# Kernel tuning notes

Hardware: AMD Instinct MI355X
Metric: run time of the kernel (lower is better)

## Reference

```python
import jax, jax.numpy as jnp
import numpy as np
from jax import lax

B, C, H, W = 32, 256, 56, 56
EPS = 1e-5


def ste_sign(x):
    # Binarize with clipped straight-through estimator (ReActNet style):
    # forward = sign(x), backward = 1 where |x| < 1.
    c = jnp.clip(x, -1.0, 1.0)
    return c + lax.stop_gradient(jnp.sign(x) - c)


def rsign(x, beta):
    # per-channel learnable shift then binarize; beta: [C]
    return ste_sign(x - beta[None, :, None, None])


def scaled_sign_weight(w):
    # w: [Cout, Cin, k, k] -> alpha * sign(w), alpha = mean|w| per filter
    alpha = jnp.mean(jnp.abs(w), axis=(1, 2, 3), keepdims=True)
    sw = w + lax.stop_gradient(jnp.sign(w) - w)  # STE through sign
    return alpha * sw


def conv2d(x, w, padding):
    return lax.conv_general_dilated(
        x, w, window_strides=(1, 1), padding=[(padding, padding)] * 2,
        dimension_numbers=("NCHW", "OIHW", "NCHW"))


def bn(x, g, b, m, v):
    inv = g / jnp.sqrt(v + EPS)
    return x * inv[None, :, None, None] + (b - m * inv)[None, :, None, None]


def rprelu(x, gamma, slope, zeta):
    # RPReLU: PReLU(x - gamma) + zeta, all per-channel
    y = x - gamma[None, :, None, None]
    return jnp.where(y > 0, y, slope[None, :, None, None] * y) + zeta[None, :, None, None]


def setup_inputs() -> dict:
    key = jax.random.key(0)
    ks = jax.random.split(key, 12)
    return {
        "x": jax.random.normal(ks[0], (B, C, H, W), jnp.float32),
        "rsign1_beta": jax.random.normal(ks[1], (C,), jnp.float32) * 0.1,
        "w1": jax.random.normal(ks[2], (C, C, 3, 3), jnp.float32) * 0.05,
        "bn1_g": jnp.ones((C,), jnp.float32),
        "bn1_b": jnp.zeros((C,), jnp.float32),
        "bn1_m": jax.random.normal(ks[3], (C,), jnp.float32) * 0.1,
        "bn1_v": jax.random.uniform(ks[4], (C,), jnp.float32) + 0.5,
        "rsign2_beta": jax.random.normal(ks[5], (C,), jnp.float32) * 0.1,
        "w2": jax.random.normal(ks[6], (C, C, 1, 1), jnp.float32) * 0.05,
        "bn2_g": jnp.ones((C,), jnp.float32),
        "bn2_b": jnp.zeros((C,), jnp.float32),
        "bn2_m": jax.random.normal(ks[7], (C,), jnp.float32) * 0.1,
        "bn2_v": jax.random.uniform(ks[8], (C,), jnp.float32) + 0.5,
        "pr_gamma": jax.random.normal(ks[9], (C,), jnp.float32) * 0.1,
        "pr_slope": jnp.full((C,), 0.25, jnp.float32),
        "pr_zeta": jax.random.normal(ks[10], (C,), jnp.float32) * 0.1,
    }


def reference(x, rsign1_beta, w1, bn1_g, bn1_b, bn1_m, bn1_v,
              rsign2_beta, w2, bn2_g, bn2_b, bn2_m, bn2_v,
              pr_gamma, pr_slope, pr_zeta):
    # layer1: RSign -> binarized 3x3 conv -> BN, + residual, RPReLU
    out = bn(conv2d(rsign(x, rsign1_beta), scaled_sign_weight(w1), 1),
             bn1_g, bn1_b, bn1_m, bn1_v)
    out = out + x
    out_r = rprelu(out, pr_gamma, pr_slope, pr_zeta)
    # layer2: RSign -> binarized 1x1 conv -> BN, + residual, RPReLU (shared params)
    out = bn(conv2d(rsign(out_r, rsign2_beta), scaled_sign_weight(w2), 0),
             bn2_g, bn2_b, bn2_m, bn2_v)
    out = out + out_r
    return rprelu(out, pr_gamma, pr_slope, pr_zeta)
```

## Files before the change

### kernel.cpp

```cpp
#include <hip/hip_runtime.h>
#include <stdint.h>

#define BB 32
#define CC_ 256
#define HH 56
#define WW 56
#define TW 28
#define TCOLS 30
#define EPSV 1e-5f

typedef unsigned long long u64;

__global__ __launch_bounds__(256) void prep_weights(
    const float* __restrict__ w1, const float* __restrict__ w2,
    const float* __restrict__ bn1_g, const float* __restrict__ bn1_b,
    const float* __restrict__ bn1_m, const float* __restrict__ bn1_v,
    const float* __restrict__ bn2_g, const float* __restrict__ bn2_b,
    const float* __restrict__ bn2_m, const float* __restrict__ bn2_v,
    u64* __restrict__ pw1, u64* __restrict__ pw2,
    float* __restrict__ scale1, float* __restrict__ shift1,
    float* __restrict__ scale2, float* __restrict__ shift2)
{
    int co = blockIdx.x;
    int ci = threadIdx.x;
    int wv = ci >> 6, lane = ci & 63;

    float wvals[9];
    const float* wp = w1 + ((size_t)co*256 + ci)*9;
    float s1 = 0.f;
#pragma unroll
    for (int t = 0; t < 9; ++t) { wvals[t] = wp[t]; s1 += fabsf(wvals[t]); }
    float v2 = w2[(size_t)co*256 + ci];
    float s2 = fabsf(v2);

#pragma unroll
    for (int t = 0; t < 9; ++t) {
        u64 b = __ballot(wvals[t] > 0.0f);
        if (lane == 0) pw1[((size_t)co*9 + t)*4 + wv] = b;
    }
    {
        u64 b = __ballot(v2 > 0.0f);
        if (lane == 0) pw2[(size_t)co*4 + wv] = b;
    }

    for (int off = 32; off > 0; off >>= 1) {
        s1 += __shfl_down(s1, off);
        s2 += __shfl_down(s2, off);
    }
    __shared__ float r1[4], r2[4];
    if (lane == 0) { r1[wv] = s1; r2[wv] = s2; }
    __syncthreads();
    if (ci == 0) {
        float a1 = (r1[0]+r1[1]+r1[2]+r1[3]) * (1.0f/2304.0f);
        float a2 = (r2[0]+r2[1]+r2[2]+r2[3]) * (1.0f/256.0f);
        float inv1 = bn1_g[co] / sqrtf(bn1_v[co] + EPSV);
        float inv2 = bn2_g[co] / sqrtf(bn2_v[co] + EPSV);
        scale1[co] = a1 * inv1;
        shift1[co] = bn1_b[co] - bn1_m[co]*inv1;
        scale2[co] = a2 * inv2;
        shift2[co] = bn2_b[co] - bn2_m[co]*inv2;
    }
}

__global__ __launch_bounds__(256) void pack_input(
    const float* __restrict__ x, const float* __restrict__ beta1,
    u64* __restrict__ pack1)
{
    __shared__ float xrow[CC_][WW+1];
    int bid = blockIdx.x;
    int n = bid / HH, h = bid % HH;
    int tid = threadIdx.x;

    for (int idx = tid; idx < CC_*14; idx += 256) {
        int c = idx / 14, g = idx - c*14;
        float4 v = *(const float4*)(x + (((size_t)n*CC_ + c)*HH + h)*WW + 4*g);
        xrow[c][4*g+0] = v.x; xrow[c][4*g+1] = v.y;
        xrow[c][4*g+2] = v.z; xrow[c][4*g+3] = v.w;
    }
    __syncthreads();

    int wv = tid >> 6, lane = tid & 63;
    float beta = beta1[wv*64 + lane];
    u64 mine = 0;
    for (int ww = 0; ww < WW; ++ww) {
        u64 b = __ballot(xrow[wv*64 + lane][ww] > beta);
        if (ww == lane) mine = b;
    }
    if (lane < WW) pack1[((size_t)bid*WW + lane)*4 + wv] = mine;
}

__device__ __forceinline__ int tap_pop(const u64* __restrict__ col, const u64* __restrict__ wr) {
    ulonglong2 a = *(const ulonglong2*)(col);
    ulonglong2 b = *(const ulonglong2*)(col + 2);
    return __builtin_popcountll(a.x ^ wr[0]) + __builtin_popcountll(a.y ^ wr[1])
         + __builtin_popcountll(b.x ^ wr[2]) + __builtin_popcountll(b.y ^ wr[3]);
}

__global__ __launch_bounds__(256, 4) void main_fused(
    const float* __restrict__ x,
    const u64* __restrict__ pack1,
    const u64* __restrict__ pw1, const u64* __restrict__ pw2,
    const float* __restrict__ scale1, const float* __restrict__ shift1,
    const float* __restrict__ scale2, const float* __restrict__ shift2,
    const float* __restrict__ beta2,
    const float* __restrict__ pr_gamma, const float* __restrict__ pr_slope,
    const float* __restrict__ pr_zeta,
    float* __restrict__ out)
{
    __shared__ u64 rows[3][TCOLS][4];
    __shared__ float outr[CC_][TW+1];
    __shared__ u64 p2[TW][4];

    int bid = blockIdx.x;
    int tile = bid & 1;
    int nh = bid >> 1;
    int n = nh / HH, h = nh % HH;
    int w0 = tile * TW;
    int tid = threadIdx.x;
    int wv = tid >> 6;
    int lane = tid & 63;
    int cc = tid;

    u64 wr1[36];
    {
        const u64* wq1 = pw1 + (size_t)cc*36;
#pragma unroll
        for (int j = 0; j < 18; ++j) {
            ulonglong2 v = *(const ulonglong2*)(wq1 + 2*j);
            wr1[2*j] = v.x; wr1[2*j+1] = v.y;
        }
    }
    u64 wr2[4];
    {
        ulonglong2 a = *(const ulonglong2*)(pw2 + (size_t)cc*4);
        ulonglong2 b = *(const ulonglong2*)(pw2 + (size_t)cc*4 + 2);
        wr2[0]=a.x; wr2[1]=a.y; wr2[2]=b.x; wr2[3]=b.y;
    }
    float sc1 = scale1[cc], sh1 = shift1[cc];
    float sc2 = scale2[cc], sh2 = shift2[cc];
    float gam = pr_gamma[cc], slp = pr_slope[cc], zet = pr_zeta[cc];
    float bet2 = beta2[cc];

    {
        int hm = (h > 0) ? h-1 : 0;
        int hp = (h < HH-1) ? h+1 : HH-1;
        for (int idx = tid; idx < 3*TCOLS*4; idx += 256) {
            int r = idx / (TCOLS*4);
            int rem = idx - r*(TCOLS*4);
            int j = rem >> 2, q = rem & 3;
            int gw = w0 - 1 + j;
            gw = (gw < 0) ? 0 : ((gw > WW-1) ? WW-1 : gw);
            int hr = (r == 0) ? hm : ((r == 1) ? h : hp);
            rows[r][j][q] = pack1[((size_t)(n*HH + hr)*WW + gw)*4 + q];
        }
    }
    for (int idx = tid; idx < CC_*7; idx += 256) {
        int c = idx / 7, g = idx - c*7;
        float4 v = *(const float4*)(x + (((size_t)n*CC_ + c)*HH + h)*WW + w0 + 4*g);
        outr[c][4*g+0] = v.x; outr[c][4*g+1] = v.y;
        outr[c][4*g+2] = v.z; outr[c][4*g+3] = v.w;
    }
    __syncthreads();

    bool rowU = (h > 0), rowD = (h < HH-1);

    if (rowU && rowD) {
        int pstart = 0, pend = TW;
        if (tile == 0) {
            int acc = 0;
#pragma unroll
            for (int r = 0; r < 3; ++r) {
                acc += tap_pop(&rows[r][1][0], &wr1[(r*3+1)*4]);
                acc += tap_pop(&rows[r][2][0], &wr1[(r*3+2)*4]);
            }
            float s = (float)(1536 - 2*acc);
            float y = fmaf(s, sc1, sh1) + outr[cc][0];
            float yr = y - gam;
            outr[cc][0] = fmaf(slp, fminf(yr, 0.f), fmaxf(yr, 0.f)) + zet;
            pstart = 1;
        } else {
            int acc = 0;
#pragma unroll
            for (int r = 0; r < 3; ++r) {
                acc += tap_pop(&rows[r][TW-1][0], &wr1[(r*3+0)*4]);
                acc += tap_pop(&rows[r][TW][0],   &wr1[(r*3+1)*4]);
            }
            float s = (float)(1536 - 2*acc);
            float y = fmaf(s, sc1, sh1) + outr[cc][TW-1];
            float yr = y - gam;
            outr[cc][TW-1] = fmaf(slp, fminf(yr, 0.f), fmaxf(yr, 0.f)) + zet;
            pend = TW-1;
        }
        for (int p = pstart; p < pend; ++p) {
            int acc = 0;
#pragma unroll
            for (int r = 0; r < 3; ++r) {
#pragma unroll
                for (int dc = 0; dc < 3; ++dc)
                    acc += tap_pop(&rows[r][p+dc][0], &wr1[(r*3+dc)*4]);
            }
            float s = (float)(2304 - 2*acc);
            float y = fmaf(s, sc1, sh1) + outr[cc][p];
            float yr = y - gam;
            outr[cc][p] = fmaf(slp, fminf(yr, 0.f), fmaxf(yr, 0.f)) + zet;
        }
    } else {
        for (int p = 0; p < TW; ++p) {
            int w = w0 + p;
            bool colL = (w > 0), colR = (w < WW-1);
            int acc = 0, nval = 0;
#pragma unroll
            for (int t = 0; t < 9; ++t) {
                int r = t / 3, dc = t - 3*r;
                bool v = ((r == 0) ? rowU : (r == 2) ? rowD : true)
                      && ((dc == 0) ? colL : (dc == 2) ? colR : true);
                if (v) { acc += tap_pop(&rows[r][p+dc][0], &wr1[t*4]); ++nval; }
            }
            float s = (float)(256*nval - 2*acc);
            float y = fmaf(s, sc1, sh1) + outr[cc][p];
            float yr = y - gam;
            outr[cc][p] = fmaf(slp, fminf(yr, 0.f), fmaxf(yr, 0.f)) + zet;
        }
    }

    {
        u64 mine = 0;
        for (int ww = 0; ww < TW; ++ww) {
            u64 b = __ballot(outr[cc][ww] > bet2);
            if (ww == lane) mine = b;
        }
        if (lane < TW) p2[lane][wv] = mine;
    }
    __syncthreads();

    for (int p = 0; p < TW; ++p) {
        ulonglong2 a = *(const ulonglong2*)&p2[p][0];
        ulonglong2 b = *(const ulonglong2*)&p2[p][2];
        int pc = __builtin_popcountll(a.x ^ wr2[0]) + __builtin_popcountll(a.y ^ wr2[1])
               + __builtin_popcountll(b.x ^ wr2[2]) + __builtin_popcountll(b.y ^ wr2[3]);
        float s = (float)(256 - 2*pc);
        float y = fmaf(s, sc2, sh2) + outr[cc][p];
        float yr = y - gam;
        outr[cc][p] = fmaf(slp, fminf(yr, 0.f), fmaxf(yr, 0.f)) + zet;
    }
    __syncthreads();

    for (int idx = tid; idx < CC_*7; idx += 256) {
        int c = idx / 7, g = idx - c*7;
        float4 v;
        v.x = outr[c][4*g+0]; v.y = outr[c][4*g+1];
        v.z = outr[c][4*g+2]; v.w = outr[c][4*g+3];
        *(float4*)(out + (((size_t)n*CC_ + c)*HH + h)*WW + w0 + 4*g) = v;
    }
}

extern "C" void kernel_launch(void* const* d_in, const int* in_sizes, int n_in,
                              void* d_out, int out_size, void* d_ws, size_t ws_size,
                              hipStream_t stream) {
    const float* x           = (const float*)d_in[0];
    const float* rsign1_beta = (const float*)d_in[1];
    const float* w1          = (const float*)d_in[2];
    const float* bn1_g       = (const float*)d_in[3];
    const float* bn1_b       = (const float*)d_in[4];
    const float* bn1_m       = (const float*)d_in[5];
    const float* bn1_v       = (const float*)d_in[6];
    const float* rsign2_beta = (const float*)d_in[7];
    const float* w2          = (const float*)d_in[8];
    const float* bn2_g       = (const float*)d_in[9];
    const float* bn2_b       = (const float*)d_in[10];
    const float* bn2_m       = (const float*)d_in[11];
    const float* bn2_v       = (const float*)d_in[12];
    const float* pr_gamma    = (const float*)d_in[13];
    const float* pr_slope    = (const float*)d_in[14];
    const float* pr_zeta     = (const float*)d_in[15];

    char* ws = (char*)d_ws;
    u64*   pw1    = (u64*)(ws);
    u64*   pw2    = (u64*)(ws + 73728);
    float* scale1 = (float*)(ws + 81920);
    float* shift1 = (float*)(ws + 82944);
    float* scale2 = (float*)(ws + 83968);
    float* shift2 = (float*)(ws + 84992);
    u64*   pack1  = (u64*)(ws + 86016);

    prep_weights<<<256, 256, 0, stream>>>(w1, w2, bn1_g, bn1_b, bn1_m, bn1_v,
                                          bn2_g, bn2_b, bn2_m, bn2_v,
                                          pw1, pw2, scale1, shift1, scale2, shift2);
    pack_input<<<BB*HH, 256, 0, stream>>>(x, rsign1_beta, pack1);
    main_fused<<<BB*HH*2, 256, 0, stream>>>(x, pack1, pw1, pw2,
                                            scale1, shift1, scale2, shift2,
                                            rsign2_beta, pr_gamma, pr_slope, pr_zeta,
                                            (float*)d_out);
}
```

Before: 381.5 us.

## Split binary 3x3 conv into two channel-half passes with register-rotated column window

The 3x3 XNOR-popcount conv now runs in two passes, each over half of the 256 input channels. Each pass keeps only 18 u64 weight words in registers instead of 36, and the 1x1 weights are loaded late, just before use. Within a pass, the three columns of the 3x3 window rotate through registers, so each LDS column is loaded once instead of three times. The first pass stores a partial sum in shared memory, and the second pass finishes BN and RPReLU. Tile-edge pixels are recomputed afterwards from a saved copy of x. The aim is to relieve register pressure and possible spilling under the 4-blocks-per-CU launch bound, at the cost of an extra read/write of the LDS output tile and more code complexity.

Measured after the change: 394.1 us. 1.03x slower.

```diff
diff --git a/kernel.cpp b/kernel.cpp
--- a/kernel.cpp
+++ b/kernel.cpp
@@ -89,12 +89,26 @@
     if (lane < WW) pack1[((size_t)bid*WW + lane)*4 + wv] = mine;
 }
 
-__device__ __forceinline__ int tap_pop(const u64* __restrict__ col, const u64* __restrict__ wr) {
-    ulonglong2 a = *(const ulonglong2*)(col);
-    ulonglong2 b = *(const ulonglong2*)(col + 2);
-    return __builtin_popcountll(a.x ^ wr[0]) + __builtin_popcountll(a.y ^ wr[1])
-         + __builtin_popcountll(b.x ^ wr[2]) + __builtin_popcountll(b.y ^ wr[3]);
-}
+#define PC2(x0,x1,w0,w1) (__builtin_popcountll((x0)^(w0)) + __builtin_popcountll((x1)^(w1)))
+
+#define ACC9(L,M,R) \
+ ( PC2(L[0],L[1],Wh[0],Wh[1])   + PC2(M[0],M[1],Wh[2],Wh[3])   + PC2(R[0],R[1],Wh[4],Wh[5]) \
+ + PC2(L[2],L[3],Wh[6],Wh[7])   + PC2(M[2],M[3],Wh[8],Wh[9])   + PC2(R[2],R[3],Wh[10],Wh[11]) \
+ + PC2(L[4],L[5],Wh[12],Wh[13]) + PC2(M[4],M[5],Wh[14],Wh[15]) + PC2(R[4],R[5],Wh[16],Wh[17]) )
+
+#define LOADCOL(D,J) do { \
+    ulonglong2 t0_ = *(const ulonglong2*)&rows[0][(J)][hi2]; \
+    ulonglong2 t1_ = *(const ulonglong2*)&rows[1][(J)][hi2]; \
+    ulonglong2 t2_ = *(const ulonglong2*)&rows[2][(J)][hi2]; \
+    D[0]=t0_.x; D[1]=t0_.y; D[2]=t1_.x; D[3]=t1_.y; D[4]=t2_.x; D[5]=t2_.y; } while(0)
+
+#define STEP(L,M,R,P) do { \
+    int acc_ = ACC9(L,M,R); \
+    float cur_ = outr[cc][(P)]; \
+    float val_ = fmaf((float)(1152 - 2*acc_), sc1, cur_); \
+    if (passB) { val_ += sh1; float yr_ = val_ - gam; \
+                 val_ = fmaf(slp, fminf(yr_,0.f), fmaxf(yr_,0.f)) + zet; } \
+    outr[cc][(P)] = val_; } while(0)
 
 __global__ __launch_bounds__(256, 4) void main_fused(
     const float* __restrict__ x,
@@ -121,25 +135,11 @@
     int lane = tid & 63;
     int cc = tid;
 
-    u64 wr1[36];
-    {
-        const u64* wq1 = pw1 + (size_t)cc*36;
-#pragma unroll
-        for (int j = 0; j < 18; ++j) {
-            ulonglong2 v = *(const ulonglong2*)(wq1 + 2*j);
-            wr1[2*j] = v.x; wr1[2*j+1] = v.y;
-        }
-    }
-    u64 wr2[4];
-    {
-        ulonglong2 a = *(const ulonglong2*)(pw2 + (size_t)cc*4);
-        ulonglong2 b = *(const ulonglong2*)(pw2 + (size_t)cc*4 + 2);
-        wr2[0]=a.x; wr2[1]=a.y; wr2[2]=b.x; wr2[3]=b.y;
-    }
     float sc1 = scale1[cc], sh1 = shift1[cc];
     float sc2 = scale2[cc], sh2 = shift2[cc];
     float gam = pr_gamma[cc], slp = pr_slope[cc], zet = pr_zeta[cc];
     float bet2 = beta2[cc];
+    const u64* wq = pw1 + (size_t)cc*36;
 
     {
         int hm = (h > 0) ? h-1 : 0;
@@ -165,61 +165,89 @@
     bool rowU = (h > 0), rowD = (h < HH-1);
 
     if (rowU && rowD) {
-        int pstart = 0, pend = TW;
+        float xe = (tile == 0) ? outr[cc][0] : outr[cc][TW-1];
+
+        for (int hi2 = 0; hi2 <= 2; hi2 += 2) {
+            bool passB = (hi2 != 0);
+            u64 Wh[18];
+#pragma unroll
+            for (int t = 0; t < 9; ++t) {
+                ulonglong2 v = *(const ulonglong2*)(wq + t*4 + hi2);
+                Wh[2*t] = v.x; Wh[2*t+1] = v.y;
+            }
+            u64 wa[6], wb[6], wc[6];
+            LOADCOL(wa, 0); LOADCOL(wb, 1);
+            int p = 0;
+            for (int it = 0; it < 9; ++it) {
+                LOADCOL(wc, p+2); STEP(wa, wb, wc, p);
+                LOADCOL(wa, p+3); STEP(wb, wc, wa, p+1);
+                LOADCOL(wb, p+4); STEP(wc, wa, wb, p+2);
+                p += 3;
+            }
+            LOADCOL(wc, 29); STEP(wa, wb, wc, 27);
+        }
+
         if (tile == 0) {
             int acc = 0;
 #pragma unroll
             for (int r = 0; r < 3; ++r) {
-                acc += tap_pop(&rows[r][1][0], &wr1[(r*3+1)*4]);
-                acc += tap_pop(&rows[r][2][0], &wr1[(r*3+2)*4]);
-            }
-            float s = (float)(1536 - 2*acc);
-            float y = fmaf(s, sc1, sh1) + outr[cc][0];
+#pragma unroll
+                for (int dc = 1; dc <= 2; ++dc) {
+                    const u64* wt = wq + (r*3+dc)*4;
+                    acc += PC2(rows[r][dc][0], rows[r][dc][1], wt[0], wt[1])
+                         + PC2(rows[r][dc][2], rows[r][dc][3], wt[2], wt[3]);
+                }
+            }
+            float y = fmaf((float)(1536 - 2*acc), sc1, sh1) + xe;
             float yr = y - gam;
-            outr[cc][0] = fmaf(slp, fminf(yr, 0.f), fmaxf(yr, 0.f)) + zet;
-            pstart = 1;
+            outr[cc][0] = fmaf(slp, fminf(yr,0.f), fmaxf(yr,0.f)) + zet;
         } else {
             int acc = 0;
 #pragma unroll
             for (int r = 0; r < 3; ++r) {
-                acc += tap_pop(&rows[r][TW-1][0], &wr1[(r*3+0)*4]);
-                acc += tap_pop(&rows[r][TW][0],   &wr1[(r*3+1)*4]);
-            }
-            float s = (float)(1536 - 2*acc);
-            float y = fmaf(s, sc1, sh1) + outr[cc][TW-1];
+#pragma unroll
+                for (int dc = 0; dc <= 1; ++dc) {
+                    const u64* wt = wq + (r*3+dc)*4;
+                    acc += PC2(rows[r][27+dc][0], rows[r][27+dc][1], wt[0], wt[1])
+                         + PC2(rows[r][27+dc][2], rows[r][27+dc][3], wt[2], wt[3]);
+                }
+            }
+            float y = fmaf((float)(1536 - 2*acc), sc1, sh1) + xe;
             float yr = y - gam;
-            outr[cc][TW-1] = fmaf(slp, fminf(yr, 0.f), fmaxf(yr, 0.f)) + zet;
-            pend = TW-1;
-        }
-        for (int p = pstart; p < pend; ++p) {
-            int acc = 0;
-#pragma unroll
-            for (int r = 0; r < 3; ++r) {
-#pragma unroll
-                for (int dc = 0; dc < 3; ++dc)
-                    acc += tap_pop(&rows[r][p+dc][0], &wr1[(r*3+dc)*4]);
-            }
-            float s = (float)(2304 - 2*acc);
-            float y = fmaf(s, sc1, sh1) + outr[cc][p];
-            float yr = y - gam;
-            outr[cc][p] = fmaf(slp, fminf(yr, 0.f), fmaxf(yr, 0.f)) + zet;
+            outr[cc][TW-1] = fmaf(slp, fminf(yr,0.f), fmaxf(yr,0.f)) + zet;
         }
     } else {
-        for (int p = 0; p < TW; ++p) {
-            int w = w0 + p;
-            bool colL = (w > 0), colR = (w < WW-1);
-            int acc = 0, nval = 0;
+        for (int hi2 = 0; hi2 <= 2; hi2 += 2) {
+            bool passB = (hi2 != 0);
+            u64 Wh[18];
 #pragma unroll
             for (int t = 0; t < 9; ++t) {
-                int r = t / 3, dc = t - 3*r;
-                bool v = ((r == 0) ? rowU : (r == 2) ? rowD : true)
-                      && ((dc == 0) ? colL : (dc == 2) ? colR : true);
-                if (v) { acc += tap_pop(&rows[r][p+dc][0], &wr1[t*4]); ++nval; }
-            }
-            float s = (float)(256*nval - 2*acc);
-            float y = fmaf(s, sc1, sh1) + outr[cc][p];
-            float yr = y - gam;
-            outr[cc][p] = fmaf(slp, fminf(yr, 0.f), fmaxf(yr, 0.f)) + zet;
+                ulonglong2 v = *(const ulonglong2*)(wq + t*4 + hi2);
+                Wh[2*t] = v.x; Wh[2*t+1] = v.y;
+            }
+            for (int p = 0; p < TW; ++p) {
+                int w = w0 + p;
+                bool colL = (w > 0), colR = (w < WW-1);
+                int acc = 0, nval = 0;
+#pragma unroll
+                for (int t = 0; t < 9; ++t) {
+                    int r = t / 3, dc = t - 3*r;
+                    bool v = ((r == 0) ? rowU : (r == 2) ? rowD : true)
+                          && ((dc == 0) ? colL : (dc == 2) ? colR : true);
+                    if (v) {
+                        acc += PC2(rows[r][p+dc][hi2], rows[r][p+dc][hi2+1],
+                                   Wh[2*t], Wh[2*t+1]);
+                        ++nval;
+                    }
+                }
+                float cur = outr[cc][p];
+                float val = fmaf((float)(128*nval - 2*acc), sc1, cur);
+                if (passB) {
+                    val += sh1; float yr = val - gam;
+                    val = fmaf(slp, fminf(yr,0.f), fmaxf(yr,0.f)) + zet;
+                }
+                outr[cc][p] = val;
+            }
         }
     }
 
@@ -233,15 +261,19 @@
     }
     __syncthreads();
 
-    for (int p = 0; p < TW; ++p) {
-        ulonglong2 a = *(const ulonglong2*)&p2[p][0];
-        ulonglong2 b = *(const ulonglong2*)&p2[p][2];
-        int pc = __builtin_popcountll(a.x ^ wr2[0]) + __builtin_popcountll(a.y ^ wr2[1])
-               + __builtin_popcountll(b.x ^ wr2[2]) + __builtin_popcountll(b.y ^ wr2[3]);
-        float s = (float)(256 - 2*pc);
-        float y = fmaf(s, sc2, sh2) + outr[cc][p];
-        float yr = y - gam;
-        outr[cc][p] = fmaf(slp, fminf(yr, 0.f), fmaxf(yr, 0.f)) + zet;
+    {
+        ulonglong2 qa = *(const ulonglong2*)(pw2 + (size_t)cc*4);
+        ulonglong2 qb = *(const ulonglong2*)(pw2 + (size_t)cc*4 + 2);
+        u64 q0 = qa.x, q1 = qa.y, q2 = qb.x, q3 = qb.y;
+        for (int p = 0; p < TW; ++p) {
+            ulonglong2 a = *(const ulonglong2*)&p2[p][0];
+            ulonglong2 b = *(const ulonglong2*)&p2[p][2];
+            int pc = PC2(a.x, a.y, q0, q1) + PC2(b.x, b.y, q2, q3);
+            float s = (float)(256 - 2*pc);
+            float y = fmaf(s, sc2, sh2) + outr[cc][p];
+            float yr = y - gam;
+            outr[cc][p] = fmaf(slp, fminf(yr,0.f), fmaxf(yr,0.f)) + zet;
+        }
     }
     __syncthreads();
 
```

## Register-rotate 3x3 binary conv columns and pin weights in scalar-named registers

Applied to the files above, without the earlier changes.

Replaces array-based weight and tap loads with explicitly named register variables pinned by empty asm. The interior pixel loop now rotates three column register sets, so each packed column is loaded from shared memory once and reused across three output pixels. Edge pixels are handled after the main sweep, and launch bounds drop to 3 waves-per-SIMD hint to allow more registers. The pw2 weights load is deferred to the second stage to shorten register live ranges. The aim is fewer LDS reads per pixel, at the cost of higher register pressure and lower occupancy.

Measured after the change: 664.5 us. 1.74x slower.

```diff
diff --git a/kernel.cpp b/kernel.cpp
--- a/kernel.cpp
+++ b/kernel.cpp
@@ -89,14 +89,41 @@
     if (lane < WW) pack1[((size_t)bid*WW + lane)*4 + wv] = mine;
 }
 
-__device__ __forceinline__ int tap_pop(const u64* __restrict__ col, const u64* __restrict__ wr) {
-    ulonglong2 a = *(const ulonglong2*)(col);
-    ulonglong2 b = *(const ulonglong2*)(col + 2);
-    return __builtin_popcountll(a.x ^ wr[0]) + __builtin_popcountll(a.y ^ wr[1])
-         + __builtin_popcountll(b.x ^ wr[2]) + __builtin_popcountll(b.y ^ wr[3]);
-}
-
-__global__ __launch_bounds__(256, 4) void main_fused(
+#define CAT3(a,b,c) a##b##c
+#define V_(S,R,Q) CAT3(S,R,Q)
+
+#define TAP(S,R,T) ( __builtin_popcountll(V_(S,R,0) ^ V_(W,T,0)) \
+                   + __builtin_popcountll(V_(S,R,1) ^ V_(W,T,1)) \
+                   + __builtin_popcountll(V_(S,R,2) ^ V_(W,T,2)) \
+                   + __builtin_popcountll(V_(S,R,3) ^ V_(W,T,3)) )
+
+#define LDW(T) do { \
+    ulonglong2 a_ = *(const ulonglong2*)(wq + (T)*4); \
+    ulonglong2 b_ = *(const ulonglong2*)(wq + (T)*4 + 2); \
+    V_(W,T,0)=a_.x; V_(W,T,1)=a_.y; V_(W,T,2)=b_.x; V_(W,T,3)=b_.y; } while(0)
+
+#define PIN(v) asm volatile("" : "+v"(v))
+
+#define CLOAD(S,J) do { \
+    ulonglong2 x0_ = *(const ulonglong2*)&rows[0][(J)][0]; \
+    ulonglong2 x1_ = *(const ulonglong2*)&rows[0][(J)][2]; \
+    ulonglong2 y0_ = *(const ulonglong2*)&rows[1][(J)][0]; \
+    ulonglong2 y1_ = *(const ulonglong2*)&rows[1][(J)][2]; \
+    ulonglong2 z0_ = *(const ulonglong2*)&rows[2][(J)][0]; \
+    ulonglong2 z1_ = *(const ulonglong2*)&rows[2][(J)][2]; \
+    V_(S,0,0)=x0_.x; V_(S,0,1)=x0_.y; V_(S,0,2)=x1_.x; V_(S,0,3)=x1_.y; \
+    V_(S,1,0)=y0_.x; V_(S,1,1)=y0_.y; V_(S,1,2)=y1_.x; V_(S,1,3)=y1_.y; \
+    V_(S,2,0)=z0_.x; V_(S,2,1)=z0_.y; V_(S,2,2)=z1_.x; V_(S,2,3)=z1_.y; } while(0)
+
+#define PIX(L,M,R_,P) do { \
+    int acc_ = TAP(L,0,0)+TAP(M,0,1)+TAP(R_,0,2) \
+             + TAP(L,1,3)+TAP(M,1,4)+TAP(R_,1,5) \
+             + TAP(L,2,6)+TAP(M,2,7)+TAP(R_,2,8); \
+    float y_ = fmaf((float)(2304 - 2*acc_), sc1, sh1) + outr[cc][(P)]; \
+    float yr_ = y_ - gam; \
+    outr[cc][(P)] = fmaf(slp, fminf(yr_,0.f), fmaxf(yr_,0.f)) + zet; } while(0)
+
+__global__ __launch_bounds__(256, 3) void main_fused(
     const float* __restrict__ x,
     const u64* __restrict__ pack1,
     const u64* __restrict__ pw1, const u64* __restrict__ pw2,
@@ -121,25 +148,21 @@
     int lane = tid & 63;
     int cc = tid;
 
-    u64 wr1[36];
-    {
-        const u64* wq1 = pw1 + (size_t)cc*36;
-#pragma unroll
-        for (int j = 0; j < 18; ++j) {
-            ulonglong2 v = *(const ulonglong2*)(wq1 + 2*j);
-            wr1[2*j] = v.x; wr1[2*j+1] = v.y;
-        }
-    }
-    u64 wr2[4];
-    {
-        ulonglong2 a = *(const ulonglong2*)(pw2 + (size_t)cc*4);
-        ulonglong2 b = *(const ulonglong2*)(pw2 + (size_t)cc*4 + 2);
-        wr2[0]=a.x; wr2[1]=a.y; wr2[2]=b.x; wr2[3]=b.y;
-    }
     float sc1 = scale1[cc], sh1 = shift1[cc];
     float sc2 = scale2[cc], sh2 = shift2[cc];
     float gam = pr_gamma[cc], slp = pr_slope[cc], zet = pr_zeta[cc];
     float bet2 = beta2[cc];
+    const u64* wq = pw1 + (size_t)cc*36;
+
+    u64 W00,W01,W02,W03, W10,W11,W12,W13, W20,W21,W22,W23;
+    u64 W30,W31,W32,W33, W40,W41,W42,W43, W50,W51,W52,W53;
+    u64 W60,W61,W62,W63, W70,W71,W72,W73, W80,W81,W82,W83;
+    LDW(0); LDW(1); LDW(2); LDW(3); LDW(4); LDW(5); LDW(6); LDW(7); LDW(8);
+    PIN(W00);PIN(W01);PIN(W02);PIN(W03); PIN(W10);PIN(W11);PIN(W12);PIN(W13);
+    PIN(W20);PIN(W21);PIN(W22);PIN(W23); PIN(W30);PIN(W31);PIN(W32);PIN(W33);
+    PIN(W40);PIN(W41);PIN(W42);PIN(W43); PIN(W50);PIN(W51);PIN(W52);PIN(W53);
+    PIN(W60);PIN(W61);PIN(W62);PIN(W63); PIN(W70);PIN(W71);PIN(W72);PIN(W73);
+    PIN(W80);PIN(W81);PIN(W82);PIN(W83);
 
     {
         int hm = (h > 0) ? h-1 : 0;
@@ -164,62 +187,62 @@
 
     bool rowU = (h > 0), rowD = (h < HH-1);
 
+    u64 A00,A01,A02,A03, A10,A11,A12,A13, A20,A21,A22,A23;
+    u64 B00,B01,B02,B03, B10,B11,B12,B13, B20,B21,B22,B23;
+    u64 C00,C01,C02,C03, C10,C11,C12,C13, C20,C21,C22,C23;
+
     if (rowU && rowD) {
-        int pstart = 0, pend = TW;
+        float xe = (tile == 0) ? outr[cc][0] : outr[cc][TW-1];
+
+        CLOAD(A,0); CLOAD(B,1);
+        int p = 0;
+        for (int it = 0; it < 9; ++it) {
+            CLOAD(C,p+2); PIX(A,B,C,p);
+            CLOAD(A,p+3); PIX(B,C,A,p+1);
+            CLOAD(B,p+4); PIX(C,A,B,p+2);
+            p += 3;
+        }
+        CLOAD(C,29); PIX(A,B,C,27);
+
         if (tile == 0) {
-            int acc = 0;
-#pragma unroll
-            for (int r = 0; r < 3; ++r) {
-                acc += tap_pop(&rows[r][1][0], &wr1[(r*3+1)*4]);
-                acc += tap_pop(&rows[r][2][0], &wr1[(r*3+2)*4]);
-            }
-            float s = (float)(1536 - 2*acc);
-            float y = fmaf(s, sc1, sh1) + outr[cc][0];
+            CLOAD(A,1); CLOAD(B,2);
+            int acc = TAP(A,0,1)+TAP(B,0,2)
+                    + TAP(A,1,4)+TAP(B,1,5)
+                    + TAP(A,2,7)+TAP(B,2,8);
+            float y = fmaf((float)(1536 - 2*acc), sc1, sh1) + xe;
             float yr = y - gam;
-            outr[cc][0] = fmaf(slp, fminf(yr, 0.f), fmaxf(yr, 0.f)) + zet;
-            pstart = 1;
+            outr[cc][0] = fmaf(slp, fminf(yr,0.f), fmaxf(yr,0.f)) + zet;
         } else {
-            int acc = 0;
-#pragma unroll
-            for (int r = 0; r < 3; ++r) {
-                acc += tap_pop(&rows[r][TW-1][0], &wr1[(r*3+0)*4]);
-                acc += tap_pop(&rows[r][TW][0],   &wr1[(r*3+1)*4]);
-            }
-            float s = (float)(1536 - 2*acc);
-            float y = fmaf(s, sc1, sh1) + outr[cc][TW-1];
+            CLOAD(A,27); CLOAD(B,28);
+            int acc = TAP(A,0,0)+TAP(B,0,1)
+                    + TAP(A,1,3)+TAP(B,1,4)
+                    + TAP(A,2,6)+TAP(B,2,7);
+            float y = fmaf((float)(1536 - 2*acc), sc1, sh1) + xe;
             float yr = y - gam;
-            outr[cc][TW-1] = fmaf(slp, fminf(yr, 0.f), fmaxf(yr, 0.f)) + zet;
-            pend = TW-1;
-        }
-        for (int p = pstart; p < pend; ++p) {
-            int acc = 0;
-#pragma unroll
-            for (int r = 0; r < 3; ++r) {
-#pragma unroll
-                for (int dc = 0; dc < 3; ++dc)
-                    acc += tap_pop(&rows[r][p+dc][0], &wr1[(r*3+dc)*4]);
-            }
-            float s = (float)(2304 - 2*acc);
-            float y = fmaf(s, sc1, sh1) + outr[cc][p];
-            float yr = y - gam;
-            outr[cc][p] = fmaf(slp, fminf(yr, 0.f), fmaxf(yr, 0.f)) + zet;
+            outr[cc][TW-1] = fmaf(slp, fminf(yr,0.f), fmaxf(yr,0.f)) + zet;
         }
     } else {
         for (int p = 0; p < TW; ++p) {
             int w = w0 + p;
             bool colL = (w > 0), colR = (w < WW-1);
+            CLOAD(A,p); CLOAD(B,p+1); CLOAD(C,p+2);
             int acc = 0, nval = 0;
-#pragma unroll
-            for (int t = 0; t < 9; ++t) {
-                int r = t / 3, dc = t - 3*r;
-                bool v = ((r == 0) ? rowU : (r == 2) ? rowD : true)
-                      && ((dc == 0) ? colL : (dc == 2) ? colR : true);
-                if (v) { acc += tap_pop(&rows[r][p+dc][0], &wr1[t*4]); ++nval; }
+            if (rowU) {
+                if (colL) { acc += TAP(A,0,0); ++nval; }
+                acc += TAP(B,0,1); ++nval;
+                if (colR) { acc += TAP(C,0,2); ++nval; }
             }
-            float s = (float)(256*nval - 2*acc);
-            float y = fmaf(s, sc1, sh1) + outr[cc][p];
+            if (colL) { acc += TAP(A,1,3); ++nval; }
+            acc += TAP(B,1,4); ++nval;
+            if (colR) { acc += TAP(C,1,5); ++nval; }
+            if (rowD) {
+                if (colL) { acc += TAP(A,2,6); ++nval; }
+                acc += TAP(B,2,7); ++nval;
+                if (colR) { acc += TAP(C,2,8); ++nval; }
+            }
+            float y = fmaf((float)(256*nval - 2*acc), sc1, sh1) + outr[cc][p];
             float yr = y - gam;
-            outr[cc][p] = fmaf(slp, fminf(yr, 0.f), fmaxf(yr, 0.f)) + zet;
+            outr[cc][p] = fmaf(slp, fminf(yr,0.f), fmaxf(yr,0.f)) + zet;
         }
     }
 
@@ -233,15 +256,20 @@
     }
     __syncthreads();
 
-    for (int p = 0; p < TW; ++p) {
-        ulonglong2 a = *(const ulonglong2*)&p2[p][0];
-        ulonglong2 b = *(const ulonglong2*)&p2[p][2];
-        int pc = __builtin_popcountll(a.x ^ wr2[0]) + __builtin_popcountll(a.y ^ wr2[1])
-               + __builtin_popcountll(b.x ^ wr2[2]) + __builtin_popcountll(b.y ^ wr2[3]);
-        float s = (float)(256 - 2*pc);
-        float y = fmaf(s, sc2, sh2) + outr[cc][p];
-        float yr = y - gam;
-        outr[cc][p] = fmaf(slp, fminf(yr, 0.f), fmaxf(yr, 0.f)) + zet;
+    {
+        ulonglong2 qa = *(const ulonglong2*)(pw2 + (size_t)cc*4);
+        ulonglong2 qb = *(const ulonglong2*)(pw2 + (size_t)cc*4 + 2);
+        u64 q0 = qa.x, q1 = qa.y, q2 = qb.x, q3 = qb.y;
+        for (int p = 0; p < TW; ++p) {
+            ulonglong2 a = *(const ulonglong2*)&p2[p][0];
+            ulonglong2 b = *(const ulonglong2*)&p2[p][2];
+            int pc = __builtin_popcountll(a.x ^ q0) + __builtin_popcountll(a.y ^ q1)
+                   + __builtin_popcountll(b.x ^ q2) + __builtin_popcountll(b.y ^ q3);
+            float s = (float)(256 - 2*pc);
+            float y = fmaf(s, sc2, sh2) + outr[cc][p];
+            float yr = y - gam;
+            outr[cc][p] = fmaf(slp, fminf(yr,0.f), fmaxf(yr,0.f)) + zet;
+        }
     }
     __syncthreads();
 
```
